# Kernel optimization log

Hardware: AMD Instinct MI355X
Metric: run time of the kernel (lower is better)

Reference implementation:

```python
import jax, jax.numpy as jnp
import numpy as np

N_EMBD = 1024
N_HEAD = 16
HEAD = N_EMBD // N_HEAD
B, T = 4, 2048


def setup_inputs() -> dict:
    key = jax.random.key(0)
    k1, k2, k3, k4, k5 = jax.random.split(key, 5)
    s = 1.0 / np.sqrt(N_EMBD)
    x = jax.random.normal(k1, (B, T, N_EMBD), dtype=jnp.float32)
    W_qkv = jax.random.uniform(k2, (N_EMBD, 3 * N_EMBD), jnp.float32, -s, s)
    b_qkv = jax.random.uniform(k3, (3 * N_EMBD,), jnp.float32, -s, s)
    W_out = jax.random.uniform(k4, (N_EMBD, N_EMBD), jnp.float32, -s, s)
    b_out = jax.random.uniform(k5, (N_EMBD,), jnp.float32, -s, s)
    return {"x": x, "W_qkv": W_qkv, "b_qkv": b_qkv, "W_out": W_out, "b_out": b_out}


def reference(x, W_qkv, b_qkv, W_out, b_out):
    Bx, Tx, C = x.shape
    qkv = x @ W_qkv + b_qkv                      # [B,T,3C]
    q, k, v = jnp.split(qkv, 3, axis=-1)
    def to_heads(t):
        return t.reshape(Bx, Tx, N_HEAD, HEAD).transpose(0, 2, 1, 3)  # [B,H,T,hd]
    q, k, v = to_heads(q), to_heads(k), to_heads(v)
    scores = jnp.einsum('bhqd,bhkd->bhqk', q, k) / np.sqrt(HEAD)
    causal = jnp.tril(jnp.ones((Tx, Tx), dtype=bool))
    scores = jnp.where(causal[None, None, :, :], scores, jnp.float32(-1e9))
    attn = jax.nn.softmax(scores, axis=-1)       # dropout p=0 (eval)
    out = jnp.einsum('bhqk,bhkd->bhqd', attn, v)
    out = out.transpose(0, 2, 1, 3).reshape(Bx, Tx, C)
    return out @ W_out + b_out
```

## Files before the change

kernel.cpp:

```cpp
#include <hip/hip_runtime.h>

typedef __attribute__((ext_vector_type(8))) short short8;
typedef __attribute__((ext_vector_type(8))) _Float16 half8;
typedef __attribute__((ext_vector_type(4))) float f32x4;

#define MFMA_BF16(a, b, c) __builtin_amdgcn_mfma_f32_16x16x32_bf16(a, b, c, 0, 0, 0)
#define MFMA_F16(a, b, c) __builtin_amdgcn_mfma_f32_16x16x32_f16(a, b, c, 0, 0, 0)

#define GLD16(g, l)                                                          \
  __builtin_amdgcn_global_load_lds(                                          \
      (const __attribute__((address_space(1))) unsigned int*)(g),            \
      (__attribute__((address_space(3))) unsigned int*)(l), 16, 0, 0)

__device__ __forceinline__ unsigned short f2bf(float f) {
  unsigned int u = __float_as_uint(f);
  u += 0x7fffu + ((u >> 16) & 1u);
  return (unsigned short)(u >> 16);
}

__global__ __launch_bounds__(256) void cvt_f32_bf16_k(const float* __restrict__ in,
                                                      unsigned short* __restrict__ out,
                                                      int n4) {
  int i = blockIdx.x * 256 + threadIdx.x;
  if (i < n4) {
    float4 v = reinterpret_cast<const float4*>(in)[i];
    ushort4 o;
    o.x = f2bf(v.x); o.y = f2bf(v.y); o.z = f2bf(v.z); o.w = f2bf(v.w);
    reinterpret_cast<ushort4*>(out)[i] = o;
  }
}

__global__ __launch_bounds__(256) void transpose_cvt_k(const float* __restrict__ W,
                                                       unsigned short* __restrict__ Wt,
                                                       int N) {
  __shared__ float tile[64][65];
  const int tid = threadIdx.x;
  const int tk = blockIdx.x * 64;
  const int tn = blockIdx.y * 64;
#pragma unroll
  for (int c = 0; c < 4; ++c) {
    int k = c * 16 + (tid >> 4);
    int n = (tid & 15) * 4;
    float4 v = *reinterpret_cast<const float4*>(&W[(size_t)(tk + k) * N + tn + n]);
    tile[k][n] = v.x; tile[k][n + 1] = v.y; tile[k][n + 2] = v.z; tile[k][n + 3] = v.w;
  }
  __syncthreads();
#pragma unroll
  for (int p = 0; p < 2; ++p) {
    int n = p * 32 + (tid >> 3);
    int k = (tid & 7) * 8;
    ushort4 a, b;
    a.x = f2bf(tile[k + 0][n]); a.y = f2bf(tile[k + 1][n]);
    a.z = f2bf(tile[k + 2][n]); a.w = f2bf(tile[k + 3][n]);
    b.x = f2bf(tile[k + 4][n]); b.y = f2bf(tile[k + 5][n]);
    b.z = f2bf(tile[k + 6][n]); b.w = f2bf(tile[k + 7][n]);
    *reinterpret_cast<ushort4*>(&Wt[(size_t)(tn + n) * 1024 + tk + k]) = a;
    *reinterpret_cast<ushort4*>(&Wt[(size_t)(tn + n) * 1024 + tk + k + 4]) = b;
  }
}

template <int MODE, int BN>
__global__ __launch_bounds__(256) void gemm_bt(const unsigned short* __restrict__ A,
                                               const unsigned short* __restrict__ Bt,
                                               const float* __restrict__ bias,
                                               float* __restrict__ outF,
                                               unsigned short* __restrict__ q_ws,
                                               unsigned short* __restrict__ k_ws,
                                               unsigned short* __restrict__ vt_ws,
                                               int M, int N, int K) {
  constexpr int NJ = BN / 32;
  constexpr int NBC = BN * 64 / 2048;
  __shared__ unsigned short As[128 * 64];
  __shared__ unsigned short Bs[BN * 64];

  const int tid = threadIdx.x;
  const int wave = tid >> 6, lane = tid & 63;
  const int quad = lane >> 4, l15 = lane & 15;
  const int m0 = blockIdx.x * 128, n0 = blockIdx.y * BN;
  const int wm = (wave & 1) * 64, wn = (wave >> 1) * (BN / 2);

  const f32x4 zf = {0.f, 0.f, 0.f, 0.f};
  f32x4 acc[4][NJ];
#pragma unroll
  for (int i = 0; i < 4; ++i)
#pragma unroll
    for (int j = 0; j < NJ; ++j) acc[i][j] = zf;

  const int rr = tid >> 3;
  const int scol = ((tid & 7) ^ (rr & 7)) * 8;
  const int swz = l15 & 7;

  for (int kt = 0; kt < K; kt += 64) {
    __syncthreads();
#pragma unroll
    for (int c = 0; c < 4; ++c)
      GLD16(&A[(size_t)(m0 + c * 32 + rr) * K + kt + scol], &As[c * 2048 + tid * 8]);
#pragma unroll
    for (int c = 0; c < NBC; ++c)
      GLD16(&Bt[(size_t)(n0 + c * 32 + rr) * K + kt + scol], &Bs[c * 2048 + tid * 8]);
    __syncthreads();

#pragma unroll
    for (int kk = 0; kk < 2; ++kk) {
      const int ch = (kk * 4 + quad) ^ swz;
      short8 af[4], bg[NJ];
#pragma unroll
      for (int i = 0; i < 4; ++i)
        af[i] = *reinterpret_cast<const short8*>(&As[(wm + i * 16 + l15) * 64 + ch * 8]);
#pragma unroll
      for (int j = 0; j < NJ; ++j)
        bg[j] = *reinterpret_cast<const short8*>(&Bs[(wn + j * 16 + l15) * 64 + ch * 8]);
#pragma unroll
      for (int i = 0; i < 4; ++i)
#pragma unroll
        for (int j = 0; j < NJ; ++j) acc[i][j] = MFMA_BF16(af[i], bg[j], acc[i][j]);
    }
  }

  const float kScQ = 0.125f * 1.44269504088896f;
  const int cls = n0 >> 10;
#pragma unroll
  for (int i = 0; i < 4; ++i) {
#pragma unroll
    for (int j = 0; j < NJ; ++j) {
      const int n = n0 + wn + j * 16 + l15;
      const float bv = bias[n];
      const int mb = m0 + wm + i * 16 + quad * 4;
      if (MODE == 1) {
#pragma unroll
        for (int r = 0; r < 4; ++r) outF[(size_t)(mb + r) * N + n] = acc[i][j][r] + bv;
      } else if (cls == 0) {
        const int b = mb >> 11, t0 = mb & 2047;
        const int h = n >> 6, d = n & 63;
#pragma unroll
        for (int r = 0; r < 4; ++r)
          q_ws[(((size_t)(b * 16 + h)) * 2048 + t0 + r) * 64 + d] =
              f2bf((acc[i][j][r] + bv) * kScQ);
      } else if (cls == 1) {
        const int b = mb >> 11, t0 = mb & 2047;
        const int n2 = n - 1024, h = n2 >> 6, d = n2 & 63;
#pragma unroll
        for (int r = 0; r < 4; ++r)
          k_ws[(((size_t)(b * 16 + h)) * 2048 + t0 + r) * 64 + d] = f2bf(acc[i][j][r] + bv);
      } else {
        const int b = mb >> 11, t0 = mb & 2047;
        const int n2 = n - 2048, h = n2 >> 6, d = n2 & 63;
        uint2 pk;
        pk.x = __builtin_bit_cast(unsigned int,
                                  __builtin_amdgcn_cvt_pkrtz(acc[i][j][0] + bv, acc[i][j][1] + bv));
        pk.y = __builtin_bit_cast(unsigned int,
                                  __builtin_amdgcn_cvt_pkrtz(acc[i][j][2] + bv, acc[i][j][3] + bv));
        *reinterpret_cast<uint2*>(
            &vt_ws[(((size_t)(b * 16 + h)) * 64 + d) * 2048 + t0]) = pk;
      }
    }
  }
}

__global__ __launch_bounds__(512, 8) void attn_k(const unsigned short* __restrict__ q_ws,
                                                 const unsigned short* __restrict__ k_ws,
                                                 const unsigned short* __restrict__ vt_ws,
                                                 unsigned short* __restrict__ att_ws) {
  const int T = 2048;
  const int bid = blockIdx.x;
  const int bh = (bid & 7) * 8 + ((bid >> 3) & 7);
  const int s = 15 - (bid >> 6);
  const int tid = threadIdx.x;
  const int wv = tid >> 6, lane = tid & 63;
  const int quad = lane >> 4, l15 = lane & 15;

  const unsigned short* Qh = q_ws + (size_t)bh * T * 64;
  const unsigned short* Kh = k_ws + (size_t)bh * T * 64;
  const _Float16* Vh = (const _Float16*)vt_ws + (size_t)bh * 64 * T;
  const int b = bh >> 4, h = bh & 15;

  __shared__ unsigned short Ks[2][64 * 64];
  __shared__ _Float16 Vs[2][64 * 64];
  __shared__ _Float16 plds_all[8][16 * 72];
  _Float16* plds = plds_all[wv];

  const int qw = s * 8 + wv;
  const int q0 = qw * 16;
  const int diagTile = qw >> 2;
  const int nk = 2 * s + 2;
  const int myq = q0 + l15;

  const short8 qb0 = *reinterpret_cast<const short8*>(&Qh[(size_t)(q0 + l15) * 64 + quad * 8]);
  const short8 qb1 = *reinterpret_cast<const short8*>(&Qh[(size_t)(q0 + l15) * 64 + 32 + quad * 8]);

  const f32x4 zf = {0.f, 0.f, 0.f, 0.f};
  f32x4 o[4];
#pragma unroll
  for (int n = 0; n < 4; ++n) o[n] = zf;
  float l_i = 0.f;

  const int srow = tid >> 3;
  const int schunk = (tid & 7) ^ (srow & 7);

  GLD16(&Kh[(size_t)srow * 64 + schunk * 8], &Ks[0][tid * 8]);
  GLD16(&Vh[(size_t)srow * T + schunk * 8], &Vs[0][tid * 8]);

  for (int kt = 0; kt < nk; ++kt) {
    const int cur = kt & 1, nxt = cur ^ 1;
    if (kt) asm volatile("s_barrier" ::: "memory");
    const int pf = (kt + 1 < nk) ? kt + 1 : nk - 1;
    GLD16(&Kh[(size_t)(pf * 64 + srow) * 64 + schunk * 8], &Ks[nxt][tid * 8]);
    GLD16(&Vh[(size_t)srow * T + pf * 64 + schunk * 8], &Vs[nxt][tid * 8]);
    asm volatile("s_waitcnt vmcnt(2)\n\ts_barrier" ::: "memory");

    if (kt <= diagTile) {
      const unsigned short* KsC = Ks[cur];
      const _Float16* VsC = Vs[cur];
      const int kb = kt * 64;
      f32x4 sc[4];
#pragma unroll
      for (int c = 0; c < 4; ++c) {
        const int r = c * 16 + l15;
        const int sl = quad ^ (r & 7);
        short8 k0 = *reinterpret_cast<const short8*>(&KsC[r * 64 + sl * 8]);
        short8 k1 = *reinterpret_cast<const short8*>(&KsC[r * 64 + (sl ^ 4) * 8]);
        sc[c] = MFMA_BF16(k1, qb1, MFMA_BF16(k0, qb0, zf));
      }
      if (kt == diagTile) {
#pragma unroll
        for (int c = 0; c < 4; ++c)
#pragma unroll
          for (int r = 0; r < 4; ++r) {
            const int key = kb + c * 16 + quad * 4 + r;
            sc[c][r] = (key > myq) ? -1e30f : sc[c][r];
          }
      }
#pragma unroll
      for (int c = 0; c < 4; ++c) {
        float p0 = exp2f(sc[c][0]);
        float p1 = exp2f(sc[c][1]);
        float p2 = exp2f(sc[c][2]);
        float p3 = exp2f(sc[c][3]);
        l_i += (p0 + p1) + (p2 + p3);
        uint2 pk;
        pk.x = __builtin_bit_cast(unsigned int, __builtin_amdgcn_cvt_pkrtz(p0, p1));
        pk.y = __builtin_bit_cast(unsigned int, __builtin_amdgcn_cvt_pkrtz(p2, p3));
        *reinterpret_cast<uint2*>(&plds[l15 * 72 + c * 16 + quad * 4]) = pk;
      }
      asm volatile("" ::: "memory");
#pragma unroll
      for (int ks = 0; ks < 2; ++ks) {
        half8 pb = *reinterpret_cast<const half8*>(&plds[l15 * 72 + ks * 32 + quad * 8]);
#pragma unroll
        for (int n = 0; n < 4; ++n) {
          const int vr = n * 16 + l15;
          const int vsl = (ks * 4 + quad) ^ (vr & 7);
          half8 vf = *reinterpret_cast<const half8*>(&VsC[vr * 64 + vsl * 8]);
          o[n] = MFMA_F16(vf, pb, o[n]);
        }
      }
      asm volatile("" ::: "memory");
    }
  }
  asm volatile("s_waitcnt vmcnt(0)" ::: "memory");

  l_i += __shfl_xor(l_i, 16);
  l_i += __shfl_xor(l_i, 32);
  const float inv = 1.f / l_i;
#pragma unroll
  for (int n = 0; n < 4; ++n) {
    uint2 ov;
    ov.x = (unsigned)f2bf(o[n][0] * inv) | ((unsigned)f2bf(o[n][1] * inv) << 16);
    ov.y = (unsigned)f2bf(o[n][2] * inv) | ((unsigned)f2bf(o[n][3] * inv) << 16);
    *reinterpret_cast<uint2*>(
        &att_ws[(size_t)(b * 2048 + q0 + l15) * 1024 + h * 64 + n * 16 + quad * 4]) = ov;
  }
}

extern "C" void kernel_launch(void* const* d_in, const int* in_sizes, int n_in,
                              void* d_out, int out_size, void* d_ws, size_t ws_size,
                              hipStream_t stream) {
  (void)in_sizes; (void)n_in; (void)out_size; (void)ws_size;
  const float* x     = (const float*)d_in[0];
  const float* W_qkv = (const float*)d_in[1];
  const float* b_qkv = (const float*)d_in[2];
  const float* W_out = (const float*)d_in[3];
  const float* b_out = (const float*)d_in[4];
  float* out = (float*)d_out;

  char* ws = (char*)d_ws;
  unsigned short* xb    = (unsigned short*)(ws);
  unsigned short* wqkvT = (unsigned short*)(ws + 16777216);
  unsigned short* woutT = (unsigned short*)(ws + 23068672);
  unsigned short* q_ws  = (unsigned short*)(ws + 25165824);
  unsigned short* k_ws  = (unsigned short*)(ws + 41943040);
  unsigned short* vt_ws = (unsigned short*)(ws + 58720256);
  unsigned short* attb  = (unsigned short*)(ws + 75497472);

  cvt_f32_bf16_k<<<8192, 256, 0, stream>>>(x, xb, 2097152);
  transpose_cvt_k<<<dim3(16, 48), 256, 0, stream>>>(W_qkv, wqkvT, 3072);
  transpose_cvt_k<<<dim3(16, 16), 256, 0, stream>>>(W_out, woutT, 1024);

  dim3 g1(64, 24);
  gemm_bt<0, 128><<<g1, 256, 0, stream>>>(xb, wqkvT, b_qkv, nullptr, q_ws, k_ws, vt_ws,
                                          8192, 3072, 1024);
  attn_k<<<1024, 512, 0, stream>>>(q_ws, k_ws, vt_ws, attb);

  dim3 g2(64, 16);
  gemm_bt<1, 64><<<g2, 256, 0, stream>>>(attb, woutT, b_out, out, nullptr, nullptr, nullptr,
                                         8192, 1024, 1024);
}
```

Baseline: 259.1 us.

## Switch attention kernel to 32x32x16 MFMA with 32-query waves, 256 threads

Rewrites the attention kernel to use 32x32x16 bf16/f16 MFMA instructions, giving each wave 32 query rows instead of 16 and using 4 waves per block instead of 8. Each thread now issues twice as many K/V global-to-LDS loads per tile. The change aims to raise MFMA throughput per instruction and cut LDS operand traffic per FLOP. In exchange it uses more accumulator registers per wave and has fewer waves to hide latency, with launch bounds changed to (256,3).

Result: faster. 243.0 us (-6.2%).

```diff
diff --git a/kernel.cpp b/kernel.cpp
--- a/kernel.cpp
+++ b/kernel.cpp
@@ -3,9 +3,11 @@
 typedef __attribute__((ext_vector_type(8))) short short8;
 typedef __attribute__((ext_vector_type(8))) _Float16 half8;
 typedef __attribute__((ext_vector_type(4))) float f32x4;
+typedef __attribute__((ext_vector_type(16))) float f32x16;
 
 #define MFMA_BF16(a, b, c) __builtin_amdgcn_mfma_f32_16x16x32_bf16(a, b, c, 0, 0, 0)
-#define MFMA_F16(a, b, c) __builtin_amdgcn_mfma_f32_16x16x32_f16(a, b, c, 0, 0, 0)
+#define MFMA32_BF16(a, b, c) __builtin_amdgcn_mfma_f32_32x32x16_bf16(a, b, c, 0, 0, 0)
+#define MFMA32_F16(a, b, c) __builtin_amdgcn_mfma_f32_32x32x16_f16(a, b, c, 0, 0, 0)
 
 #define GLD16(g, l)                                                          \
   __builtin_amdgcn_global_load_lds(                                          \
@@ -157,7 +159,7 @@
   }
 }
 
-__global__ __launch_bounds__(512, 8) void attn_k(const unsigned short* __restrict__ q_ws,
+__global__ __launch_bounds__(256, 3) void attn_k(const unsigned short* __restrict__ q_ws,
                                                  const unsigned short* __restrict__ k_ws,
                                                  const unsigned short* __restrict__ vt_ws,
                                                  unsigned short* __restrict__ att_ws) {
@@ -167,7 +169,7 @@
   const int s = 15 - (bid >> 6);
   const int tid = threadIdx.x;
   const int wv = tid >> 6, lane = tid & 63;
-  const int quad = lane >> 4, l15 = lane & 15;
+  const int L = lane & 31, hl = lane >> 5;
 
   const unsigned short* Qh = q_ws + (size_t)bh * T * 64;
   const unsigned short* Kh = k_ws + (size_t)bh * T * 64;
@@ -176,99 +178,109 @@
 
   __shared__ unsigned short Ks[2][64 * 64];
   __shared__ _Float16 Vs[2][64 * 64];
-  __shared__ _Float16 plds_all[8][16 * 72];
+  __shared__ _Float16 plds_all[4][32 * 72];
   _Float16* plds = plds_all[wv];
 
-  const int qw = s * 8 + wv;
-  const int q0 = qw * 16;
-  const int diagTile = qw >> 2;
+  const int qw = s * 4 + wv;
+  const int q0 = qw * 32;
+  const int diagTile = qw >> 1;
   const int nk = 2 * s + 2;
-  const int myq = q0 + l15;
-
-  const short8 qb0 = *reinterpret_cast<const short8*>(&Qh[(size_t)(q0 + l15) * 64 + quad * 8]);
-  const short8 qb1 = *reinterpret_cast<const short8*>(&Qh[(size_t)(q0 + l15) * 64 + 32 + quad * 8]);
-
-  const f32x4 zf = {0.f, 0.f, 0.f, 0.f};
-  f32x4 o[4];
-#pragma unroll
-  for (int n = 0; n < 4; ++n) o[n] = zf;
+  const int myq = q0 + L;
+
+  short8 qb[4];
+#pragma unroll
+  for (int kk = 0; kk < 4; ++kk)
+    qb[kk] = *reinterpret_cast<const short8*>(&Qh[(size_t)(q0 + L) * 64 + kk * 16 + hl * 8]);
+
+  f32x16 o0 = {}, o1 = {};
   float l_i = 0.f;
 
-  const int srow = tid >> 3;
-  const int schunk = (tid & 7) ^ (srow & 7);
-
-  GLD16(&Kh[(size_t)srow * 64 + schunk * 8], &Ks[0][tid * 8]);
-  GLD16(&Vh[(size_t)srow * T + schunk * 8], &Vs[0][tid * 8]);
+  const int srow8 = tid >> 3;
+  const int schunk = (tid & 7) ^ (srow8 & 7);
+
+  GLD16(&Kh[(size_t)srow8 * 64 + schunk * 8], &Ks[0][tid * 8]);
+  GLD16(&Kh[(size_t)(32 + srow8) * 64 + schunk * 8], &Ks[0][2048 + tid * 8]);
+  GLD16(&Vh[(size_t)srow8 * T + schunk * 8], &Vs[0][tid * 8]);
+  GLD16(&Vh[(size_t)(32 + srow8) * T + schunk * 8], &Vs[0][2048 + tid * 8]);
 
   for (int kt = 0; kt < nk; ++kt) {
     const int cur = kt & 1, nxt = cur ^ 1;
     if (kt) asm volatile("s_barrier" ::: "memory");
     const int pf = (kt + 1 < nk) ? kt + 1 : nk - 1;
-    GLD16(&Kh[(size_t)(pf * 64 + srow) * 64 + schunk * 8], &Ks[nxt][tid * 8]);
-    GLD16(&Vh[(size_t)srow * T + pf * 64 + schunk * 8], &Vs[nxt][tid * 8]);
-    asm volatile("s_waitcnt vmcnt(2)\n\ts_barrier" ::: "memory");
+    GLD16(&Kh[(size_t)(pf * 64 + srow8) * 64 + schunk * 8], &Ks[nxt][tid * 8]);
+    GLD16(&Kh[(size_t)(pf * 64 + 32 + srow8) * 64 + schunk * 8], &Ks[nxt][2048 + tid * 8]);
+    GLD16(&Vh[(size_t)srow8 * T + pf * 64 + schunk * 8], &Vs[nxt][tid * 8]);
+    GLD16(&Vh[(size_t)(32 + srow8) * T + pf * 64 + schunk * 8], &Vs[nxt][2048 + tid * 8]);
+    asm volatile("s_waitcnt vmcnt(4)\n\ts_barrier" ::: "memory");
 
     if (kt <= diagTile) {
       const unsigned short* KsC = Ks[cur];
       const _Float16* VsC = Vs[cur];
       const int kb = kt * 64;
-      f32x4 sc[4];
-#pragma unroll
-      for (int c = 0; c < 4; ++c) {
-        const int r = c * 16 + l15;
-        const int sl = quad ^ (r & 7);
-        short8 k0 = *reinterpret_cast<const short8*>(&KsC[r * 64 + sl * 8]);
-        short8 k1 = *reinterpret_cast<const short8*>(&KsC[r * 64 + (sl ^ 4) * 8]);
-        sc[c] = MFMA_BF16(k1, qb1, MFMA_BF16(k0, qb0, zf));
+
+      f32x16 sc0 = {}, sc1 = {};
+#pragma unroll
+      for (int kk = 0; kk < 4; ++kk) {
+        const int sl = ((kk * 2 + hl) ^ (L & 7)) * 8;
+        short8 k0 = *reinterpret_cast<const short8*>(&KsC[L * 64 + sl]);
+        short8 k1 = *reinterpret_cast<const short8*>(&KsC[(32 + L) * 64 + sl]);
+        sc0 = MFMA32_BF16(k0, qb[kk], sc0);
+        sc1 = MFMA32_BF16(k1, qb[kk], sc1);
       }
       if (kt == diagTile) {
 #pragma unroll
-        for (int c = 0; c < 4; ++c)
-#pragma unroll
-          for (int r = 0; r < 4; ++r) {
-            const int key = kb + c * 16 + quad * 4 + r;
-            sc[c][r] = (key > myq) ? -1e30f : sc[c][r];
-          }
-      }
-#pragma unroll
-      for (int c = 0; c < 4; ++c) {
-        float p0 = exp2f(sc[c][0]);
-        float p1 = exp2f(sc[c][1]);
-        float p2 = exp2f(sc[c][2]);
-        float p3 = exp2f(sc[c][3]);
-        l_i += (p0 + p1) + (p2 + p3);
-        uint2 pk;
-        pk.x = __builtin_bit_cast(unsigned int, __builtin_amdgcn_cvt_pkrtz(p0, p1));
-        pk.y = __builtin_bit_cast(unsigned int, __builtin_amdgcn_cvt_pkrtz(p2, p3));
-        *reinterpret_cast<uint2*>(&plds[l15 * 72 + c * 16 + quad * 4]) = pk;
+        for (int reg = 0; reg < 16; ++reg) {
+          const int row = (reg & 3) + 8 * (reg >> 2) + 4 * hl;
+          sc0[reg] = (kb + row > myq) ? -1e30f : sc0[reg];
+          sc1[reg] = (kb + 32 + row > myq) ? -1e30f : sc1[reg];
+        }
+      }
+#pragma unroll
+      for (int c = 0; c < 2; ++c) {
+        const f32x16& scc = c ? sc1 : sc0;
+#pragma unroll
+        for (int g = 0; g < 4; ++g) {
+          float a0 = exp2f(scc[4 * g + 0]);
+          float a1 = exp2f(scc[4 * g + 1]);
+          float a2 = exp2f(scc[4 * g + 2]);
+          float a3 = exp2f(scc[4 * g + 3]);
+          l_i += (a0 + a1) + (a2 + a3);
+          uint2 pk;
+          pk.x = __builtin_bit_cast(unsigned int, __builtin_amdgcn_cvt_pkrtz(a0, a1));
+          pk.y = __builtin_bit_cast(unsigned int, __builtin_amdgcn_cvt_pkrtz(a2, a3));
+          *reinterpret_cast<uint2*>(&plds[L * 72 + c * 32 + g * 8 + hl * 4]) = pk;
+        }
       }
       asm volatile("" ::: "memory");
-#pragma unroll
-      for (int ks = 0; ks < 2; ++ks) {
-        half8 pb = *reinterpret_cast<const half8*>(&plds[l15 * 72 + ks * 32 + quad * 8]);
-#pragma unroll
-        for (int n = 0; n < 4; ++n) {
-          const int vr = n * 16 + l15;
-          const int vsl = (ks * 4 + quad) ^ (vr & 7);
-          half8 vf = *reinterpret_cast<const half8*>(&VsC[vr * 64 + vsl * 8]);
-          o[n] = MFMA_F16(vf, pb, o[n]);
-        }
+
+#pragma unroll
+      for (int t = 0; t < 4; ++t) {
+        half8 pb = *reinterpret_cast<const half8*>(&plds[L * 72 + t * 16 + hl * 8]);
+        const int sl = ((t * 2 + hl) ^ (L & 7)) * 8;
+        half8 v0 = *reinterpret_cast<const half8*>(&VsC[L * 64 + sl]);
+        half8 v1 = *reinterpret_cast<const half8*>(&VsC[(32 + L) * 64 + sl]);
+        o0 = MFMA32_F16(v0, pb, o0);
+        o1 = MFMA32_F16(v1, pb, o1);
       }
       asm volatile("" ::: "memory");
     }
   }
   asm volatile("s_waitcnt vmcnt(0)" ::: "memory");
 
-  l_i += __shfl_xor(l_i, 16);
   l_i += __shfl_xor(l_i, 32);
   const float inv = 1.f / l_i;
 #pragma unroll
-  for (int n = 0; n < 4; ++n) {
-    uint2 ov;
-    ov.x = (unsigned)f2bf(o[n][0] * inv) | ((unsigned)f2bf(o[n][1] * inv) << 16);
-    ov.y = (unsigned)f2bf(o[n][2] * inv) | ((unsigned)f2bf(o[n][3] * inv) << 16);
-    *reinterpret_cast<uint2*>(
-        &att_ws[(size_t)(b * 2048 + q0 + l15) * 1024 + h * 64 + n * 16 + quad * 4]) = ov;
+  for (int sg = 0; sg < 2; ++sg) {
+    const f32x16& oo = sg ? o1 : o0;
+#pragma unroll
+    for (int g = 0; g < 4; ++g) {
+      const int d0 = sg * 32 + g * 8 + hl * 4;
+      uint2 ov;
+      ov.x = (unsigned)f2bf(oo[4 * g + 0] * inv) | ((unsigned)f2bf(oo[4 * g + 1] * inv) << 16);
+      ov.y = (unsigned)f2bf(oo[4 * g + 2] * inv) | ((unsigned)f2bf(oo[4 * g + 3] * inv) << 16);
+      *reinterpret_cast<uint2*>(
+          &att_ws[(size_t)(b * 2048 + q0 + L) * 1024 + h * 64 + d0]) = ov;
+    }
   }
 }
 
@@ -299,7 +311,7 @@
   dim3 g1(64, 24);
   gemm_bt<0, 128><<<g1, 256, 0, stream>>>(xb, wqkvT, b_qkv, nullptr, q_ws, k_ws, vt_ws,
                                           8192, 3072, 1024);
-  attn_k<<<1024, 512, 0, stream>>>(q_ws, k_ws, vt_ws, attb);
+  attn_k<<<1024, 256, 0, stream>>>(q_ws, k_ws, vt_ws, attb);
 
   dim3 g2(64, 16);
   gemm_bt<1, 64><<<g2, 256, 0, stream>>>(attb, woutT, b_out, out, nullptr, nullptr, nullptr,
```
